# Optimization experiments

Measured on AMD Instinct MI355X. Metric: run time of the kernel, lower is better.

## Reference

```python
import jax, jax.numpy as jnp
import numpy as np

B, C, H, W, NH = 16, 384, 28, 28, 6
S = H * W
EPS = 1e-5
SCALE = C ** -0.5  # note: original scales by dim**-0.5, not head_dim**-0.5


def setup_inputs():
    key = jax.random.key(0)
    ks = jax.random.split(key, 5)
    return {
        "x1": jax.random.normal(ks[0], (B, S, C), jnp.float32),
        "h1": H, "w1": W,
        "x2": jax.random.normal(ks[1], (B, S, C), jnp.float32),
        "h2": H, "w2": W,
        # stacked params for the 9 conv branches: q1,k1,v1,q2,k2,v2,q3,k3,v3
        "dw_w": jax.random.normal(ks[2], (9, C, 1, 3, 3), jnp.float32) * 0.1,
        "bn_gamma": jnp.ones((9, C), jnp.float32),
        "bn_beta": jnp.zeros((9, C), jnp.float32),
        "pw_w": jax.random.normal(ks[3], (9, C, C), jnp.float32) * (C ** -0.5),
        "pw_b": jnp.zeros((9, C), jnp.float32),
        "lin_w": jax.random.normal(ks[4], (9, C, C), jnp.float32) * (C ** -0.5),
    }


def _conv_branch(img, dw, g, b, pw, pwb):
    # depthwise 3x3 conv (no bias) -> train-mode BatchNorm2d -> 1x1 conv (bias)
    y = jax.lax.conv_general_dilated(
        img, dw, (1, 1), ((1, 1), (1, 1)),
        feature_group_count=img.shape[1],
        dimension_numbers=('NCHW', 'OIHW', 'NCHW'))
    mu = y.mean(axis=(0, 2, 3), keepdims=True)
    var = ((y - mu) ** 2).mean(axis=(0, 2, 3), keepdims=True)  # biased var, like torch BN
    y = (y - mu) * jax.lax.rsqrt(var + EPS) * g[None, :, None, None] + b[None, :, None, None]
    y = jnp.einsum('bchw,oc->bohw', y, pw) + pwb[None, :, None, None]
    return y.reshape(y.shape[0], y.shape[1], -1).transpose(0, 2, 1)  # b (h w) c


def _heads(x, w):
    # Linear (no bias): y = x @ w.T, then 'b t (h d) -> b h t d'
    y = jnp.einsum('btc,oc->bto', x, w)
    b, t, c = y.shape
    return y.reshape(b, t, NH, c // NH).transpose(0, 2, 1, 3)


def _attn(q, k, v):
    s = jnp.einsum('bhld,bhtd->bhlt', q, k) * SCALE
    a = jax.nn.softmax(s, axis=-1)
    o = jnp.einsum('bhlt,bhtd->bhld', a, v)
    b, h, t, d = o.shape
    # NOTE: original torch does .view(b, t, h*d) on a (b,h,t,d) tensor WITHOUT
    # transposing heads next to depth; replicate that raw reshape exactly.
    return o.reshape(b, t, h * d)


def _forward(x1, h1, w1, x2, h2, w2, dw_w, bn_gamma, bn_beta, pw_w, pw_b, lin_w):
    b, _, c = x1.shape
    i1 = x1.reshape(b, h1, w1, c).transpose(0, 3, 1, 2)  # b c h w
    i2 = x2.reshape(b, h2, w2, c).transpose(0, 3, 1, 2)
    i3 = i1 + i2
    imgs = (i1, i2, i3)
    outs = []
    for br in range(3):
        q = _conv_branch(imgs[br], dw_w[3*br+0], bn_gamma[3*br+0], bn_beta[3*br+0], pw_w[3*br+0], pw_b[3*br+0])
        k = _conv_branch(imgs[br], dw_w[3*br+1], bn_gamma[3*br+1], bn_beta[3*br+1], pw_w[3*br+1], pw_b[3*br+1])
        v = _conv_branch(imgs[br], dw_w[3*br+2], bn_gamma[3*br+2], bn_beta[3*br+2], pw_w[3*br+2], pw_b[3*br+2])
        # branch 3 reuses branch-2 Linear weights (bug in original source, replicated)
        li = 3 if br == 2 else 3 * br
        outs.append(_attn(_heads(q, lin_w[li+0]), _heads(k, lin_w[li+1]), _heads(v, lin_w[li+2])))
    return tuple(outs)


def reference(x1, h1, w1, x2, h2, w2, dw_w, bn_gamma, bn_beta, pw_w, pw_b, lin_w):
    return _forward(x1, h1, w1, x2, h2, w2, dw_w, bn_gamma, bn_beta, pw_w, pw_b, lin_w)
```

## Files before the change

### kernel.cpp

```cpp
#include <hip/hip_runtime.h>

typedef unsigned short u16;
typedef unsigned int u32;
typedef unsigned long long u64;

#define B_   16
#define C_   384
#define H_   28
#define W_   28
#define S_   784
#define NH_  6
#define HD_  64
#define BS_  (B_ * S_)
#define SCALE_ 0.05103103630798288f
#define LSC_   0.07362225484151387f
#define EPS_ 1e-5f

typedef __attribute__((ext_vector_type(8))) short bf16x8;
typedef __attribute__((ext_vector_type(4))) float f32x4;

__device__ __forceinline__ float bf2f(u16 u) {
    return __uint_as_float(((u32)u) << 16);
}
__device__ __forceinline__ u16 f2bf(float f) {
    u32 x = __float_as_uint(f);
    u32 r = (x + 0x7fffu + ((x >> 16) & 1u)) >> 16;
    return (u16)r;
}

__device__ __forceinline__ void gld16(const u16* g, u16* l) {
    __builtin_amdgcn_global_load_lds(
        (__attribute__((address_space(1))) void*)g,
        (__attribute__((address_space(3))) void*)l, 16, 0, 0);
}

__device__ __forceinline__ float exp2_fast(float x) {
    float r;
    asm("v_exp_f32 %0, %1" : "=v"(r) : "v"(x));
    return r;
}

__launch_bounds__(384)
__global__ void k_conv(const float* __restrict__ x1, const float* __restrict__ x2,
                       const float* __restrict__ dw, u16* __restrict__ y,
                       float* __restrict__ part) {
    int c = threadIdx.x;
    int id = blockIdx.x;
    int xcd = id & 7;
    int j = id >> 3;
    int p = xcd + 8 * (j / 28);
    int h = j % 28;
    int g = p / 16;
    int b = p % 16;

    const float* pa = x1 + (size_t)b * S_ * C_ + c;
    const float* pb = x2 + (size_t)b * S_ * C_ + c;

    float wt[3][9];
#pragma unroll
    for (int i = 0; i < 3; ++i)
#pragma unroll
        for (int t = 0; t < 9; ++t)
            wt[i][t] = dw[((3 * g + i) * C_ + c) * 9 + t];

    float a[3][3];
#pragma unroll
    for (int dh = 0; dh < 3; ++dh) {
        int hh = h + dh - 1;
        bool hv = (hh >= 0) && (hh < H_);
        size_t o1 = (size_t)(hh * W_ + 0) * C_;
        size_t o2 = (size_t)(hh * W_ + 1) * C_;
        float v1 = 0.f, v2 = 0.f;
        if (hv) {
            if (g == 0)      { v1 = pa[o1];           v2 = pa[o2]; }
            else if (g == 1) { v1 = pb[o1];           v2 = pb[o2]; }
            else             { v1 = pa[o1] + pb[o1];  v2 = pa[o2] + pb[o2]; }
        }
        a[dh][0] = 0.f; a[dh][1] = v1; a[dh][2] = v2;
    }

    u16* dst[3];
#pragma unroll
    for (int i = 0; i < 3; ++i)
        dst[i] = y + ((size_t)((3 * g + i) * B_ + b) * S_ + h * W_) * C_ + c;

    float sum[3] = {0.f, 0.f, 0.f}, sq[3] = {0.f, 0.f, 0.f};

    for (int w = 0; w < W_; ++w) {
#pragma unroll
        for (int i = 0; i < 3; ++i) {
            const float* W9 = wt[i];
            float acc = a[0][0]*W9[0] + a[0][1]*W9[1] + a[0][2]*W9[2]
                      + a[1][0]*W9[3] + a[1][1]*W9[4] + a[1][2]*W9[5]
                      + a[2][0]*W9[6] + a[2][1]*W9[7] + a[2][2]*W9[8];
            sum[i] += acc;
            sq[i] = fmaf(acc, acc, sq[i]);
            dst[i][w * C_] = f2bf(acc);
        }
        int wn = w + 2;
        bool wv = (wn < W_);
#pragma unroll
        for (int dh = 0; dh < 3; ++dh) {
            a[dh][0] = a[dh][1];
            a[dh][1] = a[dh][2];
            int hh = h + dh - 1;
            float v = 0.f;
            if (wv && hh >= 0 && hh < H_) {
                size_t off = (size_t)(hh * W_ + wn) * C_;
                if (g == 0)      v = pa[off];
                else if (g == 1) v = pb[off];
                else             v = pa[off] + pb[off];
            }
            a[dh][2] = v;
        }
    }
#pragma unroll
    for (int i = 0; i < 3; ++i) {
        atomicAdd(&part[((3 * g + i) * C_ + c) * 2],     sum[i]);
        atomicAdd(&part[((3 * g + i) * C_ + c) * 2 + 1], sq[i]);
    }
}

__global__ void k_stats2(const float* __restrict__ part,
                         const float* __restrict__ gamma, const float* __restrict__ beta,
                         float* __restrict__ aScale, float* __restrict__ bShift) {
    int c = threadIdx.x;
    int idx = blockIdx.x;
    float s = part[(idx * C_ + c) * 2];
    float q = part[(idx * C_ + c) * 2 + 1];
    float mean = s / (float)BS_;
    float var  = q / (float)BS_ - mean * mean;
    float a = gamma[idx * C_ + c] * rsqrtf(var + EPS_);
    aScale[idx * C_ + c] = a;
    bShift[idx * C_ + c] = beta[idx * C_ + c] - mean * a;
}

__global__ void k_wcomb(const float* __restrict__ pw, const float* __restrict__ pwb,
                        const float* __restrict__ lin,
                        const float* __restrict__ aScale, const float* __restrict__ bShift,
                        u16* __restrict__ Wcb, float* __restrict__ Bc) {
    __shared__ float red[8];
    int og = blockIdx.x;
    int idx = blockIdx.y;
    int c = threadIdx.x;
    int wave = c >> 6, lane = c & 63;
    int li = (idx < 3) ? idx : 3 + (idx % 3);
    float acc[8];
#pragma unroll
    for (int k = 0; k < 8; ++k) acc[k] = 0.f;
    const float* pwm = pw + (idx * C_) * C_ + c;
    const float* lb  = lin + ((li * C_) + og * 8) * C_;
    for (int m = 0; m < C_; ++m) {
        float pv = pwm[m * C_];
#pragma unroll
        for (int k = 0; k < 8; ++k)
            acc[k] += lb[k * C_ + m] * pv;
    }
    float aS = aScale[idx * C_ + c];
    float bS = bShift[idx * C_ + c];
    float pwbc = pwb[idx * C_ + c];
    for (int k = 0; k < 8; ++k) {
        int o = og * 8 + k;
        Wcb[(idx * C_ + o) * C_ + c] = f2bf(acc[k] * aS);
        float v = acc[k] * bS + lin[(li * C_ + o) * C_ + c] * pwbc;
#pragma unroll
        for (int msk = 1; msk < 64; msk <<= 1) v += __shfl_xor(v, msk);
        if (lane == 0) red[wave] = v;
        __syncthreads();
        if (c == 0)
            Bc[idx * C_ + o] = red[0] + red[1] + red[2] + red[3] + red[4] + red[5];
        __syncthreads();
    }
}

__launch_bounds__(256)
__global__ void k_gemm(const u16* __restrict__ y, const u16* __restrict__ Wcb,
                       const float* __restrict__ Bc, u16* __restrict__ qkv) {
    __shared__ __align__(16) u16 ldsA[2][4096];
    __shared__ __align__(16) u16 ldsB[2][4096];

    int id = blockIdx.x;
    int xcd = id & 7;
    int kb = id >> 3;
    int zz = kb / 21;
    int t  = kb % 21;
    int z  = zz * 8 + xcd;
    int by = t / 7, bx = t % 7;
    int idx = z >> 4, b = z & 15;

    int tid = threadIdx.x;
    int wave = tid >> 6;
    int lane = tid & 63;
    int lq = lane & 15;
    int quad = lane >> 4;
    int o_base = by * 128 + (wave & 1) * 64;
    int s_base_w = bx * 128 + (wave >> 1) * 64;

    const u16* ybase = y + (size_t)(idx * B_ + b) * S_ * C_;
    const u16* wbase = Wcb + (size_t)idx * C_ * C_;

    int r0 = tid >> 2;
    int qs = (tid & 3) ^ ((r0 ^ (r0 >> 2)) & 3);
    int srA0 = bx * 128 + r0;       if (srA0 > S_ - 1) srA0 = S_ - 1;
    int srA1 = bx * 128 + r0 + 64;  if (srA1 > S_ - 1) srA1 = S_ - 1;
    const u16* gA0 = ybase + (size_t)srA0 * C_ + qs * 8;
    const u16* gA1 = ybase + (size_t)srA1 * C_ + qs * 8;
    const u16* gB0 = wbase + (size_t)(by * 128 + r0) * C_ + qs * 8;
    const u16* gB1 = wbase + (size_t)(by * 128 + r0 + 64) * C_ + qs * 8;
    int lo0 = wave * 512;
    int lo1 = 2048 + wave * 512;

#define STAGE(stg, kk) do {                          \
        gld16(gA0 + (kk) * 32, &ldsA[stg][lo0]);     \
        gld16(gA1 + (kk) * 32, &ldsA[stg][lo1]);     \
        gld16(gB0 + (kk) * 32, &ldsB[stg][lo0]);     \
        gld16(gB1 + (kk) * 32, &ldsB[stg][lo1]);     \
    } while (0)

    f32x4 acc[4][4];
#pragma unroll
    for (int i = 0; i < 4; ++i)
#pragma unroll
        for (int j = 0; j < 4; ++j) acc[i][j] = (f32x4){0.f,0.f,0.f,0.f};

    STAGE(0, 0);
    __syncthreads();

    int qoff = (quad ^ ((lq ^ (lq >> 2)) & 3)) * 8;
    bf16x8 af[4], bw[4];
#pragma unroll
    for (int ks = 0; ks < 12; ++ks) {
        int cur = ks & 1;
        if (ks < 11) STAGE(cur ^ 1, ks + 1);
#pragma unroll
        for (int mt = 0; mt < 4; ++mt) {
            int sl = (wave >> 1) * 64 + mt * 16 + lq;
            __builtin_memcpy(&af[mt], &ldsA[cur][sl * 32 + qoff], 16);
        }
#pragma unroll
        for (int nt = 0; nt < 4; ++nt) {
            int ol = (wave & 1) * 64 + nt * 16 + lq;
            __builtin_memcpy(&bw[nt], &ldsB[cur][ol * 32 + qoff], 16);
        }
#pragma unroll
        for (int mt = 0; mt < 4; ++mt)
#pragma unroll
            for (int nt = 0; nt < 4; ++nt)
                acc[mt][nt] = __builtin_amdgcn_mfma_f32_16x16x32_bf16(
                    af[mt], bw[nt], acc[mt][nt], 0, 0, 0);
        __syncthreads();
    }
#undef STAGE

    float bias[4];
#pragma unroll
    for (int nt = 0; nt < 4; ++nt) bias[nt] = Bc[idx * C_ + o_base + nt * 16 + lq];
    u16* obase = qkv + ((size_t)(idx * B_ + b) * S_) * C_;
#pragma unroll
    for (int mt = 0; mt < 4; ++mt) {
#pragma unroll
        for (int r = 0; r < 4; ++r) {
            int s = s_base_w + mt * 16 + quad * 4 + r;
            if (s >= S_) continue;
            u16* row = obase + (size_t)s * C_ + o_base + lq;
#pragma unroll
            for (int nt = 0; nt < 4; ++nt)
                row[nt * 16] = f2bf(acc[mt][nt][r] + bias[nt]);
        }
    }
}

__launch_bounds__(256, 4)
__global__ void k_attn(const u16* __restrict__ qkv, float* __restrict__ out) {
    __shared__ __align__(16) u16 sm[12544];

    int id = blockIdx.x;
    int g8 = id & 7;
    int rest = id >> 3;
    int qtile = rest % 7;
    int zh = (rest / 7) * 8 + g8;
    int z = zh / 6, h = zh % 6;
    int br = z >> 4;
    int tid = threadIdx.x;
    int wave = tid >> 6;
    int lane = tid & 63;
    int lq = lane & 15;
    int quad = lane >> 4;

    int idxq = 3 * br;
    const u16* qp = qkv + (size_t)((idxq * B_ + (z & 15)) * S_) * C_ + h * HD_;
    const u16* kp = qkv + (size_t)(((idxq + 1) * B_ + (z & 15)) * S_) * C_ + h * HD_;
    const u16* vp = qkv + (size_t)(((idxq + 2) * B_ + (z & 15)) * S_) * C_ + h * HD_;

    int qbase = qtile * 128 + wave * 32;
    int qrA = qbase + lq;      if (qrA > S_ - 1) qrA = S_ - 1;
    int qrB = qbase + 16 + lq; if (qrB > S_ - 1) qrB = S_ - 1;
    const u16* qpa = qp + (size_t)qrA * C_ + quad * 8;
    const u16* qpb = qp + (size_t)qrB * C_ + quad * 8;
    bf16x8 aqA0 = *(const bf16x8*)qpa;
    bf16x8 aqA1 = *(const bf16x8*)(qpa + 32);
    bf16x8 aqB0 = *(const bf16x8*)qpb;
    bf16x8 aqB1 = *(const bf16x8*)(qpb + 32);

    f32x4 oA[4], oB[4];
#pragma unroll
    for (int i = 0; i < 4; ++i) { oA[i] = (f32x4){0.f,0.f,0.f,0.f}; oB[i] = oA[i]; }
    float rsA[4] = {0.f,0.f,0.f,0.f}, rsB[4] = {0.f,0.f,0.f,0.f};

    int t2 = (tid & 31) * 2;
    int dg = (tid >> 5) * 8;
    char* smb = (char*)sm;
    u32* pb0 = (u32*)sm + 2048 + wave * 1056;
    u32* pwr = pb0 + (quad * 4) * 66 + lq;
    const u32* prd = pb0 + lq * 66 + quad * 8;
    int sw = lq & 7;
    int vrb0 = lq * 128 + ((quad ^ sw) << 4);
    int vrb1 = lq * 128 + (((4 + quad) ^ sw) << 4);

#define VSTAGE(TG0, TG1) do {                                              \
        bf16x8 v0 = *(const bf16x8*)(vp + (size_t)(TG0) * C_ + dg);        \
        bf16x8 v1 = *(const bf16x8*)(vp + (size_t)(TG1) * C_ + dg);        \
        __syncthreads();                                                   \
        _Pragma("unroll")                                                  \
        for (int e = 0; e < 8; ++e) {                                      \
            u32 pk = (u32)(u16)v0[e] | ((u32)(u16)v1[e] << 16);            \
            *(u32*)(smb + (dg + e) * 128 + ((((t2 >> 3) ^ e)) << 4)        \
                    + ((t2 & 7) << 1)) = pk;                               \
        }                                                                  \
        __syncthreads();                                                   \
    } while (0)

    for (int ch = 0; ch < 12; ++ch) {
        int tc = ch * 64;
        VSTAGE(tc + t2, tc + t2 + 1);

#pragma unroll
        for (int tt = 0; tt < 4; ++tt) {
            const u16* kptr = kp + (size_t)(tc + tt * 16 + lq) * C_ + quad * 8;
            bf16x8 bk0 = *(const bf16x8*)kptr;
            bf16x8 bk1 = *(const bf16x8*)(kptr + 32);
            f32x4 sA = {0.f,0.f,0.f,0.f}, sB = sA;
            sA = __builtin_amdgcn_mfma_f32_16x16x32_bf16(aqA0, bk0, sA, 0, 0, 0);
            sA = __builtin_amdgcn_mfma_f32_16x16x32_bf16(aqA1, bk1, sA, 0, 0, 0);
            sB = __builtin_amdgcn_mfma_f32_16x16x32_bf16(aqB0, bk0, sB, 0, 0, 0);
            sB = __builtin_amdgcn_mfma_f32_16x16x32_bf16(aqB1, bk1, sB, 0, 0, 0);
#pragma unroll
            for (int r = 0; r < 4; ++r) {
                float ea = exp2_fast(sA[r] * LSC_);
                float eb = exp2_fast(sB[r] * LSC_);
                u32 ua = __float_as_uint(ea) & 0xFFFF0000u;
                u32 ub = __float_as_uint(eb) & 0xFFFF0000u;
                rsA[r] += __uint_as_float(ua);
                rsB[r] += __uint_as_float(ub);
                pwr[r * 66 + tt * 16] = __builtin_amdgcn_perm(
                    __float_as_uint(eb), __float_as_uint(ea), 0x07060302u);
            }
        }

        bf16x8 apA[2], apB[2];
#pragma unroll
        for (int n = 0; n < 2; ++n) {
            u32 uu[8];
            __builtin_memcpy(uu, prd + n * 32, 32);
            union { u32 w[4]; bf16x8 v; } ca, cb;
#pragma unroll
            for (int jj = 0; jj < 4; ++jj) {
                ca.w[jj] = __builtin_amdgcn_perm(uu[2*jj+1], uu[2*jj], 0x05040100u);
                cb.w[jj] = __builtin_amdgcn_perm(uu[2*jj+1], uu[2*jj], 0x07060302u);
            }
            apA[n] = ca.v; apB[n] = cb.v;
        }

#pragma unroll
        for (int dt = 0; dt < 4; ++dt) {
            bf16x8 bv0, bv1;
            __builtin_memcpy(&bv0, smb + dt * 2048 + vrb0, 16);
            __builtin_memcpy(&bv1, smb + dt * 2048 + vrb1, 16);
            oA[dt] = __builtin_amdgcn_mfma_f32_16x16x32_bf16(apA[0], bv0, oA[dt], 0, 0, 0);
            oB[dt] = __builtin_amdgcn_mfma_f32_16x16x32_bf16(apB[0], bv0, oB[dt], 0, 0, 0);
            oA[dt] = __builtin_amdgcn_mfma_f32_16x16x32_bf16(apA[1], bv1, oA[dt], 0, 0, 0);
            oB[dt] = __builtin_amdgcn_mfma_f32_16x16x32_bf16(apB[1], bv1, oB[dt], 0, 0, 0);
        }
    }

    {
        int tc = 768;
        int tg0 = tc + t2;     if (tg0 > S_ - 1) tg0 = S_ - 1;
        int tg1 = tc + t2 + 1; if (tg1 > S_ - 1) tg1 = S_ - 1;
        VSTAGE(tg0, tg1);

        const u16* kptr = kp + (size_t)(tc + lq) * C_ + quad * 8;
        bf16x8 bk0 = *(const bf16x8*)kptr;
        bf16x8 bk1 = *(const bf16x8*)(kptr + 32);
        f32x4 sA = {0.f,0.f,0.f,0.f}, sB = sA;
        sA = __builtin_amdgcn_mfma_f32_16x16x32_bf16(aqA0, bk0, sA, 0, 0, 0);
        sA = __builtin_amdgcn_mfma_f32_16x16x32_bf16(aqA1, bk1, sA, 0, 0, 0);
        sB = __builtin_amdgcn_mfma_f32_16x16x32_bf16(aqB0, bk0, sB, 0, 0, 0);
        sB = __builtin_amdgcn_mfma_f32_16x16x32_bf16(aqB1, bk1, sB, 0, 0, 0);
#pragma unroll
        for (int r = 0; r < 4; ++r) {
            float ea = exp2_fast(sA[r] * LSC_);
            float eb = exp2_fast(sB[r] * LSC_);
            u32 ua = __float_as_uint(ea) & 0xFFFF0000u;
            u32 ub = __float_as_uint(eb) & 0xFFFF0000u;
            rsA[r] += __uint_as_float(ua);
            rsB[r] += __uint_as_float(ub);
            pwr[r * 66]      = __builtin_amdgcn_perm(
                __float_as_uint(eb), __float_as_uint(ea), 0x07060302u);
            pwr[r * 66 + 16] = 0;
        }

        bf16x8 apA0, apB0;
        {
            u32 uu[8];
            __builtin_memcpy(uu, prd, 32);
            union { u32 w[4]; bf16x8 v; } ca, cb;
#pragma unroll
            for (int jj = 0; jj < 4; ++jj) {
                ca.w[jj] = __builtin_amdgcn_perm(uu[2*jj+1], uu[2*jj], 0x05040100u);
                cb.w[jj] = __builtin_amdgcn_perm(uu[2*jj+1], uu[2*jj], 0x07060302u);
            }
            apA0 = ca.v; apB0 = cb.v;
        }
#pragma unroll
        for (int dt = 0; dt < 4; ++dt) {
            bf16x8 bv0;
            __builtin_memcpy(&bv0, smb + dt * 2048 + vrb0, 16);
            oA[dt] = __builtin_amdgcn_mfma_f32_16x16x32_bf16(apA0, bv0, oA[dt], 0, 0, 0);
            oB[dt] = __builtin_amdgcn_mfma_f32_16x16x32_bf16(apB0, bv0, oB[dt], 0, 0, 0);
        }
    }
#undef VSTAGE

#pragma unroll
    for (int msk = 1; msk <= 8; msk <<= 1)
#pragma unroll
        for (int r = 0; r < 4; ++r) {
            rsA[r] += __shfl_xor(rsA[r], msk);
            rsB[r] += __shfl_xor(rsB[r], msk);
        }

    size_t obase = ((size_t)z * NH_ + h) * S_ * HD_;
#pragma unroll
    for (int r = 0; r < 4; ++r) {
        int qa = qbase + quad * 4 + r;
        if (qa < S_) {
            float inv = 1.f / rsA[r];
            float* dst = out + obase + (size_t)qa * HD_ + lq;
            dst[0]  = oA[0][r] * inv;
            dst[16] = oA[1][r] * inv;
            dst[32] = oA[2][r] * inv;
            dst[48] = oA[3][r] * inv;
        }
        int qb = qbase + 16 + quad * 4 + r;
        if (qb < S_) {
            float inv = 1.f / rsB[r];
            float* dst = out + obase + (size_t)qb * HD_ + lq;
            dst[0]  = oB[0][r] * inv;
            dst[16] = oB[1][r] * inv;
            dst[32] = oB[2][r] * inv;
            dst[48] = oB[3][r] * inv;
        }
    }
}

extern "C" void kernel_launch(void* const* d_in, const int* in_sizes, int n_in,
                              void* d_out, int out_size, void* d_ws, size_t ws_size,
                              hipStream_t stream) {
    (void)in_sizes; (void)n_in; (void)out_size; (void)ws_size;
    const float* x1    = (const float*)d_in[0];
    const float* x2    = (const float*)d_in[3];
    const float* dw    = (const float*)d_in[6];
    const float* gamma = (const float*)d_in[7];
    const float* beta  = (const float*)d_in[8];
    const float* pw    = (const float*)d_in[9];
    const float* pwb   = (const float*)d_in[10];
    const float* lin   = (const float*)d_in[11];
    float* out = (float*)d_out;

    char* ws = (char*)d_ws;
    u16*  y   = (u16*)(ws + 28901376);
    u16*  qkv = (u16*)(ws + 115605504);
    u16*  Wcb = (u16*)(ws + 202309632);
    float* Bc = (float*)(ws + 204963840);
    float* aS = (float*)(ws + 204977664);
    float* bS = (float*)(ws + 204991488);
    float* part = (float*)(ws + 205005312);

    hipMemsetAsync(part, 0, 9 * C_ * 2 * sizeof(float), stream);
    k_conv  <<<dim3(1344), 384, 0, stream>>>(x1, x2, dw, y, part);
    k_stats2<<<dim3(9), 384, 0, stream>>>(part, gamma, beta, aS, bS);
    k_wcomb <<<dim3(48, 9), 384, 0, stream>>>(pw, pwb, lin, aS, bS, Wcb, Bc);
    k_gemm  <<<dim3(3024), 256, 0, stream>>>(y, Wcb, Bc, qkv);
    k_attn  <<<dim3(2016), 256, 0, stream>>>(qkv, out);
}
```

Measured before the change: 440.1 us.

## Fold BN stats into weight-combine kernel, split conv blocks, prefetch pw loads

Removes the separate k_stats2 launch by computing the BN scale and shift inside k_wcomb directly from the atomic partial sums. The depthwise conv kernel is split into three 128-thread blocks per row instead of one 384-thread block, giving more and smaller blocks. k_wcomb now uses a 1D grid with XCD-aware mapping and software-prefetches pw values in groups of 8. The stats work is repeated by every wcomb block, and the smaller conv blocks each redo their own index setup.

```diff
diff --git a/kernel.cpp b/kernel.cpp
--- a/kernel.cpp
+++ b/kernel.cpp
@@ -40,18 +40,20 @@
     return r;
 }
 
-__launch_bounds__(384)
+__launch_bounds__(128)
 __global__ void k_conv(const float* __restrict__ x1, const float* __restrict__ x2,
                        const float* __restrict__ dw, u16* __restrict__ y,
                        float* __restrict__ part) {
-    int c = threadIdx.x;
     int id = blockIdx.x;
     int xcd = id & 7;
-    int j = id >> 3;
-    int p = xcd + 8 * (j / 28);
-    int h = j % 28;
+    int r = id >> 3;
+    int cc = r % 3;
+    int rr = r / 3;
+    int p = xcd + 8 * (rr / 28);
+    int h = rr % 28;
     int g = p / 16;
     int b = p % 16;
+    int c = cc * 128 + threadIdx.x;
 
     const float* pa = x1 + (size_t)b * S_ * C_ + c;
     const float* pb = x2 + (size_t)b * S_ * C_ + c;
@@ -121,43 +123,58 @@
     }
 }
 
-__global__ void k_stats2(const float* __restrict__ part,
-                         const float* __restrict__ gamma, const float* __restrict__ beta,
-                         float* __restrict__ aScale, float* __restrict__ bShift) {
-    int c = threadIdx.x;
-    int idx = blockIdx.x;
-    float s = part[(idx * C_ + c) * 2];
-    float q = part[(idx * C_ + c) * 2 + 1];
-    float mean = s / (float)BS_;
-    float var  = q / (float)BS_ - mean * mean;
-    float a = gamma[idx * C_ + c] * rsqrtf(var + EPS_);
-    aScale[idx * C_ + c] = a;
-    bShift[idx * C_ + c] = beta[idx * C_ + c] - mean * a;
-}
-
 __global__ void k_wcomb(const float* __restrict__ pw, const float* __restrict__ pwb,
                         const float* __restrict__ lin,
-                        const float* __restrict__ aScale, const float* __restrict__ bShift,
+                        const float* __restrict__ part,
+                        const float* __restrict__ gamma, const float* __restrict__ beta,
                         u16* __restrict__ Wcb, float* __restrict__ Bc) {
     __shared__ float red[8];
-    int og = blockIdx.x;
-    int idx = blockIdx.y;
+    int id = blockIdx.x;
+    int xcd = id & 7;
+    int k2 = id >> 3;
+    int idx, og;
+    if (k2 < 48) { idx = xcd; og = k2; }
+    else         { idx = 8;   og = xcd * 6 + (k2 - 48); }
     int c = threadIdx.x;
     int wave = c >> 6, lane = c & 63;
     int li = (idx < 3) ? idx : 3 + (idx % 3);
+
+    float s_ = part[(idx * C_ + c) * 2];
+    float q_ = part[(idx * C_ + c) * 2 + 1];
+    float mean = s_ / (float)BS_;
+    float var  = q_ / (float)BS_ - mean * mean;
+    float aS = gamma[idx * C_ + c] * rsqrtf(var + EPS_);
+    float bS = beta[idx * C_ + c] - mean * aS;
+
     float acc[8];
 #pragma unroll
     for (int k = 0; k < 8; ++k) acc[k] = 0.f;
     const float* pwm = pw + (idx * C_) * C_ + c;
     const float* lb  = lin + ((li * C_) + og * 8) * C_;
-    for (int m = 0; m < C_; ++m) {
-        float pv = pwm[m * C_];
-#pragma unroll
-        for (int k = 0; k < 8; ++k)
-            acc[k] += lb[k * C_ + m] * pv;
-    }
-    float aS = aScale[idx * C_ + c];
-    float bS = bShift[idx * C_ + c];
+
+    float pvv[8];
+#pragma unroll
+    for (int u = 0; u < 8; ++u) pvv[u] = pwm[u * C_];
+    for (int m0 = 0; m0 < C_; m0 += 8) {
+        float pvn[8];
+        if (m0 + 8 < C_) {
+#pragma unroll
+            for (int u = 0; u < 8; ++u) pvn[u] = pwm[(m0 + 8 + u) * C_];
+        } else {
+#pragma unroll
+            for (int u = 0; u < 8; ++u) pvn[u] = 0.f;
+        }
+#pragma unroll
+        for (int u = 0; u < 8; ++u) {
+            float pv = pvv[u];
+#pragma unroll
+            for (int k = 0; k < 8; ++k)
+                acc[k] += lb[k * C_ + (m0 + u)] * pv;
+        }
+#pragma unroll
+        for (int u = 0; u < 8; ++u) pvv[u] = pvn[u];
+    }
+
     float pwbc = pwb[idx * C_ + c];
     for (int k = 0; k < 8; ++k) {
         int o = og * 8 + k;
@@ -483,14 +500,11 @@
     u16*  qkv = (u16*)(ws + 115605504);
     u16*  Wcb = (u16*)(ws + 202309632);
     float* Bc = (float*)(ws + 204963840);
-    float* aS = (float*)(ws + 204977664);
-    float* bS = (float*)(ws + 204991488);
     float* part = (float*)(ws + 205005312);
 
     hipMemsetAsync(part, 0, 9 * C_ * 2 * sizeof(float), stream);
-    k_conv  <<<dim3(1344), 384, 0, stream>>>(x1, x2, dw, y, part);
-    k_stats2<<<dim3(9), 384, 0, stream>>>(part, gamma, beta, aS, bS);
-    k_wcomb <<<dim3(48, 9), 384, 0, stream>>>(pw, pwb, lin, aS, bS, Wcb, Bc);
+    k_conv  <<<dim3(4032), 128, 0, stream>>>(x1, x2, dw, y, part);
+    k_wcomb <<<dim3(432), 384, 0, stream>>>(pw, pwb, lin, part, gamma, beta, Wcb, Bc);
     k_gemm  <<<dim3(3024), 256, 0, stream>>>(y, Wcb, Bc, qkv);
     k_attn  <<<dim3(2016), 256, 0, stream>>>(qkv, out);
 }
```

Result: no change. 435.9 us (-0.9%).
